# Kernel optimization log

Hardware: AMD Instinct MI355X
Metric: run time of the kernel (lower is better)

## Reference

```python
import jax, jax.numpy as jnp
import numpy as np

EPS = 1e-5

def grid_sample_bilinear(img, grid):
    """torch F.grid_sample, mode='bilinear', padding_mode='zeros', align_corners=True.
    img: (b, c, H, W); grid: (b, Hg, Wg, 2) with (x, y) in [-1, 1]. Returns (b, c, Hg, Wg)."""
    H, W = img.shape[2], img.shape[3]
    x = (grid[..., 0] + 1.0) * 0.5 * (W - 1)
    y = (grid[..., 1] + 1.0) * 0.5 * (H - 1)
    x0 = jnp.floor(x); y0 = jnp.floor(y)
    x1 = x0 + 1.0;     y1 = y0 + 1.0
    wx1 = x - x0; wx0 = 1.0 - wx1
    wy1 = y - y0; wy0 = 1.0 - wy1

    def sample_one(img_b, yi, xi):
        # img_b: (c,H,W); yi, xi: (Hg,Wg) float corner coords
        valid = ((yi >= 0) & (yi < H) & (xi >= 0) & (xi < W)).astype(img_b.dtype)
        yc = jnp.clip(yi, 0, H - 1).astype(jnp.int32)
        xc = jnp.clip(xi, 0, W - 1).astype(jnp.int32)
        return img_b[:, yc, xc] * valid[None]  # (c,Hg,Wg)

    def per_batch(img_b, x0b, x1b, y0b, y1b, wx0b, wx1b, wy0b, wy1b):
        v = (sample_one(img_b, y0b, x0b) * (wy0b * wx0b)[None]
             + sample_one(img_b, y0b, x1b) * (wy0b * wx1b)[None]
             + sample_one(img_b, y1b, x0b) * (wy1b * wx0b)[None]
             + sample_one(img_b, y1b, x1b) * (wy1b * wx1b)[None])
        return v

    return jax.vmap(per_batch)(img, x0, x1, y0, y1, wx0, wx1, wy0, wy1)


def conv_bn_relu(x, w, gamma, beta):
    # 1x1 conv (no bias) + BatchNorm2d (batch stats, training-mode forward) + ReLU
    y = jnp.einsum('nchw,oc->nohw', x, w)
    mean = y.mean(axis=(0, 2, 3), keepdims=True)
    var = y.var(axis=(0, 2, 3), keepdims=True)
    y = (y - mean) * jax.lax.rsqrt(var + EPS)
    y = y * gamma[None, :, None, None] + beta[None, :, None, None]
    return jax.nn.relu(y)


def setup_inputs() -> dict:
    key = jax.random.key(0)
    ks = jax.random.split(key, 10)
    b, c, h, w, r = 1, 128, 64, 128, 4
    d = 2 * r + 1
    f1 = jax.random.normal(ks[0], (b, c, h, w), dtype=jnp.float32)
    f2 = jax.random.normal(ks[1], (b, c, h, w), dtype=jnp.float32)
    # coords: base pixel grid (x, y) plus a small random flow perturbation
    gy, gx = jnp.meshgrid(jnp.arange(h, dtype=jnp.float32), jnp.arange(w, dtype=jnp.float32), indexing='ij')
    base = jnp.stack([gx, gy], axis=0)[None]  # (1,2,h,w)
    coords = base + 2.0 * jax.random.normal(ks[2], (b, 2, h, w), dtype=jnp.float32)
    c1, c2, c3 = 96, 128, 64
    w1 = jax.random.normal(ks[3], (c1, 2 * c), dtype=jnp.float32) * 0.05
    w2 = jax.random.normal(ks[4], (c2, c1), dtype=jnp.float32) * 0.05
    w3 = jax.random.normal(ks[5], (c3, c2), dtype=jnp.float32) * 0.05
    w4 = jax.random.normal(ks[6], (1, c3), dtype=jnp.float32) * 0.05
    b4 = jnp.zeros((1,), dtype=jnp.float32)
    g1 = jnp.ones((c1,), jnp.float32); be1 = jnp.zeros((c1,), jnp.float32)
    g2 = jnp.ones((c2,), jnp.float32); be2 = jnp.zeros((c2,), jnp.float32)
    g3 = jnp.ones((c3,), jnp.float32); be3 = jnp.zeros((c3,), jnp.float32)
    # DAP: identity init + small noise so gradients are non-trivial
    wdap = jnp.eye(d * d, dtype=jnp.float32) + 0.01 * jax.random.normal(ks[7], (d * d, d * d), dtype=jnp.float32)
    return {"f1": f1, "f2": f2, "coords": coords,
            "w1": w1, "g1": g1, "be1": be1,
            "w2": w2, "g2": g2, "be2": be2,
            "w3": w3, "g3": g3, "be3": be3,
            "w4": w4, "b4": b4, "wdap": wdap, "radius": 4}


def reference(f1, f2, coords, w1, g1, be1, w2, g2, be2, w3, g3, be3, w4, b4, wdap, radius):
    b, c, h, w = f1.shape
    r = radius
    d = 2 * r + 1
    dx = jnp.linspace(-r, r, d, dtype=f1.dtype)
    delta = jnp.stack(jnp.meshgrid(dx, dx, indexing='ij'), axis=-1)  # (d,d,2)
    coords_p = jnp.transpose(coords, (0, 2, 3, 1))  # (b,h,w,2)
    cent = coords_p[:, None, :, None, :, :] + delta.reshape(1, d, 1, d, 1, 2)  # (b,d,h,d,w,2)
    cx = 2.0 * cent[..., 0] / (w - 1) - 1.0
    cy = 2.0 * cent[..., 1] / (h - 1) - 1.0
    grid = jnp.stack([cx, cy], axis=-1).reshape(b, d * h, d * w, 2)
    f2s = grid_sample_bilinear(f2, grid)                     # (b,c,d*h,d*w)
    f2s = f2s.reshape(b, c, d, h, d, w).transpose(0, 2, 4, 1, 3, 5)  # (b,d,d,c,h,w)
    f1e = jnp.broadcast_to(f1[:, None, None], (b, d, d, c, h, w))
    corr = jnp.concatenate([f1e, f2s], axis=3).reshape(b * d * d, 2 * c, h, w)
    x = conv_bn_relu(corr, w1, g1, be1)
    x = conv_bn_relu(x, w2, g2, be2)
    x = conv_bn_relu(x, w3, g3, be3)
    cost = jnp.einsum('nchw,oc->nohw', x, w4) + b4[None, :, None, None]  # (b*d*d,1,h,w)
    cost = cost.reshape(b, d * d, h, w)
    # DAP: 1x1 conv over the d*d displacement channels, no bias
    cost = jnp.einsum('bkhw,lk->blhw', cost, wdap)
    return cost  # (b, (2r+1)^2, h, w)
```

## Files before the change

### kernel.cpp

```cpp
#include <hip/hip_runtime.h>
#include <hip/hip_bf16.h>

#define H 64
#define W 128
#define P 8192
#define DD 81
#define NS 663552
#define C1 96
#define C2 128
#define C3 64
#define EPSF 1e-5f
#define NSLOT 128

#define X1S 104
#define X2S 136
#define X1TS 136

#define NGB 324
#define NGSLOT 8

typedef __attribute__((ext_vector_type(8))) short bf16x8;
typedef __attribute__((ext_vector_type(4))) float f32x4;

#define S1SUM 0
#define S1SSQ (S1SUM + NSLOT * C1)
#define M1SUM (S1SSQ + NSLOT * C1)
#define S3SUM (M1SUM + NSLOT * C1)
#define S3SSQ (S3SUM + NSLOT * C3)
#define GSLOT (S3SSQ + NSLOT * C3)
#define STATS_ZERO_FLOATS (GSLOT + NGSLOT * 9216)
#define S1Sc 126976
#define S1Tc (S1Sc + C1)
#define S2Sc (S1Tc + C1)
#define S2Tc (S2Sc + C2)
#define S3Sc (S2Tc + C2)
#define S3Tc (S3Sc + C3)
#define GOFF 127552
#define COST_OFF (GOFF + 9216)
#define FLOAT_END (COST_OFF + NS)
#define A_BYTE   ((size_t)FLOAT_END * 4)
#define G_BYTE   (A_BYTE + (size_t)P * 96 * 2)
#define W2BF_BYTE (G_BYTE + (size_t)P * 96 * 2)
#define W3BF_BYTE (W2BF_BYTE + (size_t)C2 * C1 * 2)
#define Y1_BYTE  (W3BF_BYTE + (size_t)C3 * C2 * 2)
#define Y3_BYTE  (Y1_BYTE + (size_t)NS * C1 * 2)
#define WS_NEEDED (Y3_BYTE + (size_t)NS * C3 * 2)

__device__ __forceinline__ float bflo(unsigned u) { return __uint_as_float(u << 16); }
__device__ __forceinline__ float bfhi(unsigned u) { return __uint_as_float(u & 0xffff0000u); }
__device__ __forceinline__ float bfu(unsigned short v) { return __uint_as_float((unsigned)v << 16); }

__device__ __forceinline__ unsigned pkbf(float a, float b) {
  __hip_bfloat162 h = __float22bfloat162_rn(make_float2(a, b));
  unsigned u; __builtin_memcpy(&u, &h, 4);
  return u;
}

__global__ __launch_bounds__(256) void k_prep(const float* __restrict__ f1,
                                              const float* __restrict__ f2,
                                              const float* __restrict__ w1,
                                              unsigned short* __restrict__ aT,
                                              unsigned short* __restrict__ gT) {
  __shared__ float tile[128][64];
  int t = threadIdx.x;
  int p0 = blockIdx.x * 64;
  int px = t & 63, q = t >> 6;
  int c0 = q * 24;
  for (int pass = 0; pass < 2; ++pass) {
    const float* src = pass ? f2 : f1;
    unsigned short* dst = pass ? gT : aT;
    int koff = pass ? 128 : 0;
    __syncthreads();
    for (int idx = t; idx < 8192; idx += 256) {
      int kk = idx >> 6, xx = idx & 63;
      tile[kk][xx] = src[kk * P + p0 + xx];
    }
    __syncthreads();
    float acc[24];
#pragma unroll
    for (int i = 0; i < 24; ++i) acc[i] = 0.f;
    for (int kk = 0; kk < 128; ++kk) {
      float fv = tile[kk][px];
#pragma unroll
      for (int i = 0; i < 24; ++i)
        acc[i] += w1[(c0 + i) * 256 + koff + kk] * fv;
    }
#pragma unroll
    for (int i = 0; i < 24; i += 4) {
      uint2 pk;
      pk.x = pkbf(acc[i + 0], acc[i + 1]);
      pk.y = pkbf(acc[i + 2], acc[i + 3]);
      *(uint2*)(dst + ((size_t)((c0 + i) >> 2) * P + p0 + px) * 4) = pk;
    }
  }
}

__global__ void k_wprep(const float* __restrict__ w2, const float* __restrict__ w3,
                        unsigned short* __restrict__ w2bf, unsigned short* __restrict__ w3bf) {
  int idx = blockIdx.x * 256 + threadIdx.x;
  if (idx < C2 * C1) {
    w2bf[idx] = (unsigned short)(pkbf(w2[idx], 0.f) & 0xffffu);
  } else if (idx < C2 * C1 + C3 * C2) {
    w3bf[idx - C2 * C1] = (unsigned short)(pkbf(w3[idx - C2 * C1], 0.f) & 0xffffu);
  }
}

__global__ __launch_bounds__(256) void k_sample(const float* __restrict__ coords,
                                                float* __restrict__ ws,
                                                const unsigned short* __restrict__ aT,
                                                const unsigned short* __restrict__ gT,
                                                unsigned short* __restrict__ y1T) {
  int t = threadIdx.x, b = blockIdx.x;
  int cg = b % 6;
  int ptile = b / 6;
  int c = cg * 4 + (t >> 6);
  int px = t & 63;
  int p = ptile * 64 + px;
  float cx = coords[p], cy = coords[P + p];
  float fx0 = floorf(cx), fy0 = floorf(cy);
  float wx1 = cx - fx0, wx0 = 1.f - wx1;
  float wy1 = cy - fy0, wy0 = 1.f - wy1;
  int ixb = (int)fx0 - 4, iyb = (int)fy0 - 4;
  int colOff[10];
  float vx[10];
#pragma unroll
  for (int j = 0; j < 10; ++j) {
    int ix = ixb + j;
    vx[j] = (ix >= 0 && ix < W) ? 1.f : 0.f;
    colOff[j] = min(max(ix, 0), W - 1);
  }
  float ewx0[9], ewx1[9];
#pragma unroll
  for (int j = 0; j < 9; ++j) { ewx0[j] = wx0 * vx[j]; ewx1[j] = wx1 * vx[j + 1]; }
  int rowOff[10];
  float vy[10];
#pragma unroll
  for (int dy = 0; dy < 10; ++dy) {
    int iy = iyb + dy;
    vy[dy] = (iy >= 0 && iy < H) ? 1.f : 0.f;
    rowOff[dy] = min(max(iy, 0), H - 1) * W;
  }
  float ewy0[9], ewy1[9];
#pragma unroll
  for (int d = 0; d < 9; ++d) { ewy0[d] = wy0 * vy[d]; ewy1[d] = wy1 * vy[d + 1]; }
  float av[4];
  {
    uint2 a2 = *(const uint2*)(aT + ((size_t)c * P + p) * 4);
    av[0] = bflo(a2.x); av[1] = bfhi(a2.x); av[2] = bflo(a2.y); av[3] = bfhi(a2.y);
  }
  const unsigned short* gc = gT + (size_t)c * P * 4;
  float Hb[2][9][4];
  float sum[4] = {0.f, 0.f, 0.f, 0.f}, ssq[4] = {0.f, 0.f, 0.f, 0.f};
#pragma unroll
  for (int dy = 0; dy < 10; ++dy) {
    const int cur = dy & 1, prv = cur ^ 1;
    uint2 gv[10];
    const unsigned short* grow = gc + (size_t)rowOff[dy] * 4;
#pragma unroll
    for (int j = 0; j < 10; ++j) gv[j] = *(const uint2*)(grow + colOff[j] * 4);
#pragma unroll
    for (int j = 0; j < 9; ++j) {
      Hb[cur][j][0] = fmaf(ewx1[j], bflo(gv[j + 1].x), ewx0[j] * bflo(gv[j].x));
      Hb[cur][j][1] = fmaf(ewx1[j], bfhi(gv[j + 1].x), ewx0[j] * bfhi(gv[j].x));
      Hb[cur][j][2] = fmaf(ewx1[j], bflo(gv[j + 1].y), ewx0[j] * bflo(gv[j].y));
      Hb[cur][j][3] = fmaf(ewx1[j], bfhi(gv[j + 1].y), ewx0[j] * bfhi(gv[j].y));
    }
    if (dy >= 1) {
      const int dyk = dy - 1;
      float e0 = ewy0[dyk], e1 = ewy1[dyk];
#pragma unroll
      for (int j = 0; j < 9; ++j) {
        float o0 = fmaf(e0, Hb[prv][j][0], fmaf(e1, Hb[cur][j][0], av[0]));
        float o1 = fmaf(e0, Hb[prv][j][1], fmaf(e1, Hb[cur][j][1], av[1]));
        float o2 = fmaf(e0, Hb[prv][j][2], fmaf(e1, Hb[cur][j][2], av[2]));
        float o3 = fmaf(e0, Hb[prv][j][3], fmaf(e1, Hb[cur][j][3], av[3]));
        sum[0] += o0; ssq[0] = fmaf(o0, o0, ssq[0]);
        sum[1] += o1; ssq[1] = fmaf(o1, o1, ssq[1]);
        sum[2] += o2; ssq[2] = fmaf(o2, o2, ssq[2]);
        sum[3] += o3; ssq[3] = fmaf(o3, o3, ssq[3]);
        uint2 pk;
        pk.x = pkbf(o0, o1);
        pk.y = pkbf(o2, o3);
        int kk = j * 9 + dyk;
        *(uint2*)(y1T + (((size_t)kk * 24 + c) * P + p) * 4) = pk;
      }
    }
  }
#pragma unroll
  for (int m = 1; m < 64; m <<= 1) {
#pragma unroll
    for (int e = 0; e < 4; ++e) {
      sum[e] += __shfl_xor(sum[e], m);
      ssq[e] += __shfl_xor(ssq[e], m);
    }
  }
  if ((t & 63) == 0) {
    int slot = b & (NSLOT - 1);
#pragma unroll
    for (int e = 0; e < 4; ++e) {
      atomicAdd(&ws[S1SUM + slot * C1 + c * 4 + e], sum[e]);
      atomicAdd(&ws[S1SSQ + slot * C1 + c * 4 + e], ssq[e]);
    }
  }
}

__global__ void k_finalize(float* __restrict__ ws, int sumO, int ssqO,
                           const float* __restrict__ gamma, const float* __restrict__ beta,
                           int sO, int tO, int C) {
  int c = threadIdx.x;
  if (c < C) {
    float su = 0.f, sq = 0.f;
    for (int s = 0; s < NSLOT; ++s) { su += ws[sumO + s * C + c]; sq += ws[ssqO + s * C + c]; }
    float mean = su * (1.0f / (float)NS);
    float var = sq * (1.0f / (float)NS) - mean * mean;
    float sc = gamma[c] * rsqrtf(var + EPSF);
    ws[sO + c] = sc;
    ws[tO + c] = beta[c] - mean * sc;
  }
}

__global__ __launch_bounds__(256) void k_gram(const unsigned short* __restrict__ y1T,
                                              float* __restrict__ ws) {
  __shared__ unsigned short x1t[96 * X1TS];
  int t = threadIdx.x, b = blockIdx.x;
  int w = t >> 6, l = t & 63;
  int lr = l & 15, lh = l >> 4;
  int i0 = (w >> 1) * 48, j0 = (w & 1) * 48;
  f32x4 acc[9];
  f32x4 zero4 = {0.f, 0.f, 0.f, 0.f};
#pragma unroll
  for (int q = 0; q < 9; ++q) acc[q] = zero4;
  int c = t >> 3, pg = t & 7;
  float s1v[4], t1v[4];
  if (c < 24) {
#pragma unroll
    for (int e = 0; e < 4; ++e) { s1v[e] = ws[S1Sc + c * 4 + e]; t1v[e] = ws[S1Tc + c * 4 + e]; }
  }
  float msum[4] = {0.f, 0.f, 0.f, 0.f};
  for (int it = 0; it < 16; ++it) {
    int idx = b * 16 + it;
    int k = idx >> 6, p0 = (idx & 63) << 7;
    const unsigned short* y1k = y1T + (size_t)k * P * 96;
    __syncthreads();
    if (c < 24) {
      int pbase = p0 + pg * 16;
      unsigned rowu[4][8];
#pragma unroll
      for (int ii = 0; ii < 8; ++ii) {
        uint4 v = *(const uint4*)(y1k + ((size_t)c * P + pbase + ii * 2) * 4);
        float x00 = fmaxf(0.f, fmaf(s1v[0], bflo(v.x), t1v[0]));
        float x10 = fmaxf(0.f, fmaf(s1v[1], bfhi(v.x), t1v[1]));
        float x20 = fmaxf(0.f, fmaf(s1v[2], bflo(v.y), t1v[2]));
        float x30 = fmaxf(0.f, fmaf(s1v[3], bfhi(v.y), t1v[3]));
        float x01 = fmaxf(0.f, fmaf(s1v[0], bflo(v.z), t1v[0]));
        float x11 = fmaxf(0.f, fmaf(s1v[1], bfhi(v.z), t1v[1]));
        float x21 = fmaxf(0.f, fmaf(s1v[2], bflo(v.w), t1v[2]));
        float x31 = fmaxf(0.f, fmaf(s1v[3], bfhi(v.w), t1v[3]));
        msum[0] += x00 + x01; msum[1] += x10 + x11;
        msum[2] += x20 + x21; msum[3] += x30 + x31;
        rowu[0][ii] = pkbf(x00, x01);
        rowu[1][ii] = pkbf(x10, x11);
        rowu[2][ii] = pkbf(x20, x21);
        rowu[3][ii] = pkbf(x30, x31);
      }
#pragma unroll
      for (int e = 0; e < 4; ++e) {
        unsigned short* dst = x1t + (c * 4 + e) * X1TS + pg * 16;
        uint4 pk0; pk0.x = rowu[e][0]; pk0.y = rowu[e][1]; pk0.z = rowu[e][2]; pk0.w = rowu[e][3];
        uint4 pk1; pk1.x = rowu[e][4]; pk1.y = rowu[e][5]; pk1.z = rowu[e][6]; pk1.w = rowu[e][7];
        *(uint4*)dst = pk0;
        *(uint4*)(dst + 8) = pk1;
      }
    }
    __syncthreads();
#pragma unroll
    for (int kk = 0; kk < 4; ++kk) {
      bf16x8 a3[3], b3[3];
#pragma unroll
      for (int a = 0; a < 3; ++a)
        a3[a] = *(const bf16x8*)(const void*)(x1t + (i0 + a * 16 + lr) * X1TS + kk * 32 + lh * 8);
#pragma unroll
      for (int bb = 0; bb < 3; ++bb)
        b3[bb] = *(const bf16x8*)(const void*)(x1t + (j0 + bb * 16 + lr) * X1TS + kk * 32 + lh * 8);
#pragma unroll
      for (int a = 0; a < 3; ++a)
#pragma unroll
        for (int bb = 0; bb < 3; ++bb)
          acc[a * 3 + bb] = __builtin_amdgcn_mfma_f32_16x16x32_bf16(a3[a], b3[bb], acc[a * 3 + bb], 0, 0, 0);
    }
  }
  {
    float* gp = ws + GSLOT + (b & (NGSLOT - 1)) * 9216;
#pragma unroll
    for (int a = 0; a < 3; ++a)
#pragma unroll
      for (int bb = 0; bb < 3; ++bb) {
        int ti = (w >> 1) * 3 + a, tj = (w & 1) * 3 + bb;
        f32x4 v = acc[a * 3 + bb];
#pragma unroll
        for (int r = 0; r < 4; ++r)
          atomicAdd(&gp[(ti * 16 + lh * 4 + r) * 96 + tj * 16 + lr], v[r]);
      }
  }
  if (c < 24) {
#pragma unroll
    for (int m = 1; m < 8; m <<= 1)
#pragma unroll
      for (int e = 0; e < 4; ++e) msum[e] += __shfl_xor(msum[e], m);
    if (pg == 0) {
      int slot = b & (NSLOT - 1);
#pragma unroll
      for (int e = 0; e < 4; ++e) atomicAdd(&ws[M1SUM + slot * C1 + c * 4 + e], msum[e]);
    }
  }
}

__global__ void k_greduce(float* __restrict__ ws) {
  int e = blockIdx.x * 256 + threadIdx.x;
  float s = 0.f;
#pragma unroll
  for (int g = 0; g < NGSLOT; ++g) s += ws[GSLOT + g * 9216 + e];
  ws[GOFF + e] = s;
}

__global__ __launch_bounds__(256) void k_fin2g(float* __restrict__ ws,
                                               const unsigned short* __restrict__ w2bf,
                                               const float* __restrict__ g2,
                                               const float* __restrict__ be2) {
  __shared__ float wrow[96];
  __shared__ float m1f[96];
  __shared__ float red[8];
  int o = blockIdx.x, t = threadIdx.x;
  if (t < 96) {
    wrow[t] = bfu(w2bf[o * 96 + t]);
    float s = 0.f;
    for (int sl = 0; sl < NSLOT; ++sl) s += ws[M1SUM + sl * C1 + t];
    m1f[t] = s;
  }
  __syncthreads();
  float quad = 0.f;
  for (int e = t; e < 9216; e += 256) {
    int i = e / 96, j = e - i * 96;
    quad = fmaf(wrow[i] * wrow[j], ws[GOFF + e], quad);
  }
  float msm = (t < 96) ? wrow[t] * m1f[t] : 0.f;
#pragma unroll
  for (int m = 1; m < 64; m <<= 1) { quad += __shfl_xor(quad, m); msm += __shfl_xor(msm, m); }
  if ((t & 63) == 0) { red[t >> 6] = quad; red[4 + (t >> 6)] = msm; }
  __syncthreads();
  if (t == 0) {
    float q = red[0] + red[1] + red[2] + red[3];
    float mm = red[4] + red[5] + red[6] + red[7];
    float mean = mm * (1.0f / (float)NS);
    float var = q * (1.0f / (float)NS) - mean * mean;
    float sc = g2[o] * rsqrtf(var + EPSF);
    ws[S2Sc + o] = sc;
    ws[S2Tc + o] = be2[o] - mean * sc;
  }
}

__device__ __forceinline__ void build_x1(const unsigned short* __restrict__ y1k,
                                         const float* __restrict__ ws,
                                         unsigned short* lds, int p0, int t) {
  int s = t >> 1, hh = t & 1;
  int p = p0 + s;
  const float* s1p = ws + S1Sc;
  const float* t1p = ws + S1Tc;
  unsigned short* base = lds + s * X1S + hh * 48;
#pragma unroll
  for (int i2 = 0; i2 < 6; ++i2) {
    int c0 = hh * 12 + i2 * 2;
    uint2 va = *(const uint2*)(y1k + ((size_t)c0 * P + p) * 4);
    uint2 vb = *(const uint2*)(y1k + ((size_t)(c0 + 1) * P + p) * 4);
    int cb = c0 * 4;
    float x0 = fmaxf(0.f, fmaf(s1p[cb + 0], bflo(va.x), t1p[cb + 0]));
    float x1 = fmaxf(0.f, fmaf(s1p[cb + 1], bfhi(va.x), t1p[cb + 1]));
    float x2 = fmaxf(0.f, fmaf(s1p[cb + 2], bflo(va.y), t1p[cb + 2]));
    float x3 = fmaxf(0.f, fmaf(s1p[cb + 3], bfhi(va.y), t1p[cb + 3]));
    float x4 = fmaxf(0.f, fmaf(s1p[cb + 4], bflo(vb.x), t1p[cb + 4]));
    float x5 = fmaxf(0.f, fmaf(s1p[cb + 5], bfhi(vb.x), t1p[cb + 5]));
    float x6 = fmaxf(0.f, fmaf(s1p[cb + 6], bflo(vb.y), t1p[cb + 6]));
    float x7 = fmaxf(0.f, fmaf(s1p[cb + 7], bfhi(vb.y), t1p[cb + 7]));
    uint4 pk;
    pk.x = pkbf(x0, x1); pk.y = pkbf(x2, x3); pk.z = pkbf(x4, x5); pk.w = pkbf(x6, x7);
    *(uint4*)(base + i2 * 8) = pk;
  }
}

__global__ __launch_bounds__(256) void k_l23(const unsigned short* __restrict__ y1T,
                                             float* __restrict__ ws,
                                             const unsigned short* __restrict__ w2bf,
                                             const unsigned short* __restrict__ w3bf,
                                             unsigned short* __restrict__ y3T) {
  __shared__ unsigned short ldss[128 * X1S];
  int t = threadIdx.x, b = blockIdx.x;
  int k = b >> 6, p0 = (b & 63) << 7;
  size_t n0 = (size_t)k * P + p0;
  int slot = b & (NSLOT - 1);
  const unsigned short* y1k = y1T + (size_t)k * P * 96;
  build_x1(y1k, ws, ldss, p0, t);
  __syncthreads();
  int l = t & 63, wv = t >> 6;
  int o0w = wv * 32;
  int lr = l & 15, lh = l >> 4;
  bf16x8 af[2][3];
#pragma unroll
  for (int m = 0; m < 2; ++m)
#pragma unroll
    for (int kk = 0; kk < 3; ++kk)
      af[m][kk] = *(const bf16x8*)(const void*)(w2bf + (size_t)(o0w + m * 16 + lr) * 96 + kk * 32 + lh * 8);
  f32x4 acc[2][8];
  f32x4 zero4 = {0.f, 0.f, 0.f, 0.f};
#pragma unroll
  for (int m = 0; m < 2; ++m)
#pragma unroll
    for (int n = 0; n < 8; ++n) acc[m][n] = zero4;
#pragma unroll
  for (int kk = 0; kk < 3; ++kk)
#pragma unroll
    for (int n = 0; n < 8; ++n) {
      bf16x8 bfr = *(const bf16x8*)(const void*)(ldss + (n * 16 + lr) * X1S + kk * 32 + lh * 8);
      acc[0][n] = __builtin_amdgcn_mfma_f32_16x16x32_bf16(af[0][kk], bfr, acc[0][n], 0, 0, 0);
      acc[1][n] = __builtin_amdgcn_mfma_f32_16x16x32_bf16(af[1][kk], bfr, acc[1][n], 0, 0, 0);
    }
  float s2v[2][4], t2v[2][4];
#pragma unroll
  for (int m = 0; m < 2; ++m)
#pragma unroll
    for (int r = 0; r < 4; ++r) {
      int cc = o0w + m * 16 + lh * 4 + r;
      s2v[m][r] = ws[S2Sc + cc];
      t2v[m][r] = ws[S2Tc + cc];
    }
  int o2 = wv * 16;
  int ch4 = wv * 4 + lh;
  bf16x8 af2[4];
#pragma unroll
  for (int kk = 0; kk < 4; ++kk)
    af2[kk] = *(const bf16x8*)(const void*)(w3bf + (size_t)(o2 + lr) * 128 + kk * 32 + lh * 8);
  unsigned short* x2s = ldss;
  float ssum[4] = {0.f, 0.f, 0.f, 0.f}, sssq[4] = {0.f, 0.f, 0.f, 0.f};
#pragma unroll
  for (int h = 0; h < 2; ++h) {
    __syncthreads();
#pragma unroll
    for (int m = 0; m < 2; ++m)
#pragma unroll
      for (int n2 = 0; n2 < 4; ++n2) {
        f32x4 v = acc[m][h * 4 + n2];
        float x0 = fmaxf(0.f, fmaf(s2v[m][0], v[0], t2v[m][0]));
        float x1v = fmaxf(0.f, fmaf(s2v[m][1], v[1], t2v[m][1]));
        float x2v = fmaxf(0.f, fmaf(s2v[m][2], v[2], t2v[m][2]));
        float x3 = fmaxf(0.f, fmaf(s2v[m][3], v[3], t2v[m][3]));
        uint2 pk;
        pk.x = pkbf(x0, x1v);
        pk.y = pkbf(x2v, x3);
        *(uint2*)(x2s + (n2 * 16 + lr) * X2S + o0w + m * 16 + lh * 4) = pk;
      }
    __syncthreads();
    f32x4 acc2[4];
#pragma unroll
    for (int n2 = 0; n2 < 4; ++n2) acc2[n2] = zero4;
#pragma unroll
    for (int kk = 0; kk < 4; ++kk)
#pragma unroll
      for (int n2 = 0; n2 < 4; ++n2) {
        bf16x8 bfr = *(const bf16x8*)(const void*)(x2s + (n2 * 16 + lr) * X2S + kk * 32 + lh * 8);
        acc2[n2] = __builtin_amdgcn_mfma_f32_16x16x32_bf16(af2[kk], bfr, acc2[n2], 0, 0, 0);
      }
#pragma unroll
    for (int n2 = 0; n2 < 4; ++n2) {
      f32x4 v = acc2[n2];
#pragma unroll
      for (int r = 0; r < 4; ++r) { float x = v[r]; ssum[r] += x; sssq[r] = fmaf(x, x, sssq[r]); }
      uint2 pk;
      pk.x = pkbf(v[0], v[1]);
      pk.y = pkbf(v[2], v[3]);
      size_t n = n0 + h * 64 + n2 * 16 + lr;
      *(uint2*)(y3T + ((size_t)ch4 * NS + n) * 4) = pk;
    }
  }
#pragma unroll
  for (int msk = 1; msk < 16; msk <<= 1)
#pragma unroll
    for (int i = 0; i < 4; ++i) { ssum[i] += __shfl_xor(ssum[i], msk); sssq[i] += __shfl_xor(sssq[i], msk); }
  if (lr == 0) {
#pragma unroll
    for (int r = 0; r < 4; ++r) {
      int o = o2 + lh * 4 + r;
      atomicAdd(&ws[S3SUM + slot * C3 + o], ssum[r]);
      atomicAdd(&ws[S3SSQ + slot * C3 + o], sssq[r]);
    }
  }
}

__global__ __launch_bounds__(256) void k_layer4(const unsigned short* __restrict__ y3T,
                                                float* __restrict__ ws,
                                                const float* __restrict__ w4,
                                                const float* __restrict__ b4) {
  size_t n = (size_t)blockIdx.x * 256 + threadIdx.x;
  const float* s3p = ws + S3Sc;
  const float* t3p = ws + S3Tc;
  float acc = 0.f;
#pragma unroll
  for (int c16 = 0; c16 < 16; ++c16) {
    uint2 v = *(const uint2*)(y3T + ((size_t)c16 * NS + n) * 4);
    int c = c16 * 4;
    acc += fmaxf(0.f, fmaf(s3p[c + 0], bflo(v.x), t3p[c + 0])) * w4[c + 0];
    acc += fmaxf(0.f, fmaf(s3p[c + 1], bfhi(v.x), t3p[c + 1])) * w4[c + 1];
    acc += fmaxf(0.f, fmaf(s3p[c + 2], bflo(v.y), t3p[c + 2])) * w4[c + 2];
    acc += fmaxf(0.f, fmaf(s3p[c + 3], bfhi(v.y), t3p[c + 3])) * w4[c + 3];
  }
  ws[COST_OFF + n] = acc + b4[0];
}

__global__ __launch_bounds__(256) void k_dap(const float* __restrict__ ws,
                                             const float* __restrict__ wdap,
                                             float* __restrict__ out) {
  __shared__ float wd[DD * DD];
  int t = threadIdx.x;
  for (int i = t; i < DD * DD; i += 256) wd[i] = wdap[i];
  __syncthreads();
  int p = blockIdx.x * 32 + (t & 31);
  int lg = t >> 5;
  const float* cost = ws + COST_OFF;
  float cr[81];
#pragma unroll
  for (int kk = 0; kk < 81; ++kk) cr[kk] = cost[kk * P + p];
  for (int l = lg; l < 81; l += 8) {
    float acc = 0.f;
#pragma unroll
    for (int kk = 0; kk < 81; ++kk) acc = fmaf(wd[l * 81 + kk], cr[kk], acc);
    out[(size_t)l * P + p] = acc;
  }
}

__global__ void k_marker(float* out) { out[0] = 1.0e30f; }

extern "C" void kernel_launch(void* const* d_in, const int* in_sizes, int n_in,
                              void* d_out, int out_size, void* d_ws, size_t ws_size,
                              hipStream_t stream) {
  const float* f1 = (const float*)d_in[0];
  const float* f2 = (const float*)d_in[1];
  const float* coords = (const float*)d_in[2];
  const float* w1 = (const float*)d_in[3];
  const float* g1 = (const float*)d_in[4];
  const float* be1 = (const float*)d_in[5];
  const float* w2 = (const float*)d_in[6];
  const float* g2 = (const float*)d_in[7];
  const float* be2 = (const float*)d_in[8];
  const float* w3 = (const float*)d_in[9];
  const float* g3 = (const float*)d_in[10];
  const float* be3 = (const float*)d_in[11];
  const float* w4 = (const float*)d_in[12];
  const float* b4 = (const float*)d_in[13];
  const float* wdap = (const float*)d_in[14];
  float* out = (float*)d_out;
  float* ws = (float*)d_ws;

  if (ws_size < WS_NEEDED) {
    k_marker<<<1, 1, 0, stream>>>(out);
    return;
  }
  unsigned short* aT = (unsigned short*)((char*)d_ws + A_BYTE);
  unsigned short* gT = (unsigned short*)((char*)d_ws + G_BYTE);
  unsigned short* w2bf = (unsigned short*)((char*)d_ws + W2BF_BYTE);
  unsigned short* w3bf = (unsigned short*)((char*)d_ws + W3BF_BYTE);
  unsigned short* y1T = (unsigned short*)((char*)d_ws + Y1_BYTE);
  unsigned short* y3T = (unsigned short*)((char*)d_ws + Y3_BYTE);

  hipMemsetAsync(d_ws, 0, (size_t)STATS_ZERO_FLOATS * 4, stream);
  k_prep<<<128, 256, 0, stream>>>(f1, f2, w1, aT, gT);
  k_wprep<<<80, 256, 0, stream>>>(w2, w3, w2bf, w3bf);
  k_sample<<<768, 256, 0, stream>>>(coords, ws, aT, gT, y1T);
  k_finalize<<<1, 128, 0, stream>>>(ws, S1SUM, S1SSQ, g1, be1, S1Sc, S1Tc, C1);
  k_gram<<<NGB, 256, 0, stream>>>(y1T, ws);
  k_greduce<<<36, 256, 0, stream>>>(ws);
  k_fin2g<<<128, 256, 0, stream>>>(ws, w2bf, g2, be2);
  k_l23<<<5184, 256, 0, stream>>>(y1T, ws, w2bf, w3bf, y3T);
  k_finalize<<<1, 128, 0, stream>>>(ws, S3SUM, S3SSQ, g3, be3, S3Sc, S3Tc, C3);
  k_layer4<<<2592, 256, 0, stream>>>(y3T, ws, w4, b4);
  k_dap<<<256, 256, 0, stream>>>(ws, wdap, out);
}
```

Baseline: 294.1 us.

## Fuse layer4 into DAP kernel, split sample channels finer, quadruple gram blocks

Merges the final 64-to-1 projection into the DAP kernel, so the cost map goes through shared memory and is never written to or read back from global workspace. k_sample now handles two channels per thread instead of four and launches twice as many blocks with a launch-bounds occupancy hint. This cuts register pressure, at the price of narrower 4-byte gathers and stores. k_gram is launched with four times as many blocks, each doing a quarter of the iterations, to improve parallelism. The fused DAP kernel uses only 256 blocks to read all of y3T, which may under-occupy the GPU compared with the old 2592-block layer4 kernel.

```diff
diff --git a/kernel.cpp b/kernel.cpp
--- a/kernel.cpp
+++ b/kernel.cpp
@@ -16,7 +16,7 @@
 #define X2S 136
 #define X1TS 136
 
-#define NGB 324
+#define NGB 1296
 #define NGSLOT 8
 
 typedef __attribute__((ext_vector_type(8))) short bf16x8;
@@ -36,8 +36,7 @@
 #define S3Sc (S2Tc + C2)
 #define S3Tc (S3Sc + C3)
 #define GOFF 127552
-#define COST_OFF (GOFF + 9216)
-#define FLOAT_END (COST_OFF + NS)
+#define FLOAT_END (GOFF + 9216)
 #define A_BYTE   ((size_t)FLOAT_END * 4)
 #define G_BYTE   (A_BYTE + (size_t)P * 96 * 2)
 #define W2BF_BYTE (G_BYTE + (size_t)P * 96 * 2)
@@ -105,15 +104,16 @@
   }
 }
 
-__global__ __launch_bounds__(256) void k_sample(const float* __restrict__ coords,
-                                                float* __restrict__ ws,
-                                                const unsigned short* __restrict__ aT,
-                                                const unsigned short* __restrict__ gT,
-                                                unsigned short* __restrict__ y1T) {
+__global__ __launch_bounds__(256, 4) void k_sample(const float* __restrict__ coords,
+                                                   float* __restrict__ ws,
+                                                   const unsigned short* __restrict__ aT,
+                                                   const unsigned short* __restrict__ gT,
+                                                   unsigned short* __restrict__ y1T) {
   int t = threadIdx.x, b = blockIdx.x;
-  int cg = b % 6;
-  int ptile = b / 6;
-  int c = cg * 4 + (t >> 6);
+  int c2g = b % 12;
+  int ptile = b / 12;
+  int c2 = c2g * 4 + (t >> 6);
+  int c4 = c2 >> 1, hl = c2 & 1;
   int px = t & 63;
   int p = ptile * 64 + px;
   float cx = coords[p], cy = coords[P + p];
@@ -132,75 +132,56 @@
   float ewx0[9], ewx1[9];
 #pragma unroll
   for (int j = 0; j < 9; ++j) { ewx0[j] = wx0 * vx[j]; ewx1[j] = wx1 * vx[j + 1]; }
-  int rowOff[10];
-  float vy[10];
-#pragma unroll
-  for (int dy = 0; dy < 10; ++dy) {
-    int iy = iyb + dy;
-    vy[dy] = (iy >= 0 && iy < H) ? 1.f : 0.f;
-    rowOff[dy] = min(max(iy, 0), H - 1) * W;
-  }
-  float ewy0[9], ewy1[9];
-#pragma unroll
-  for (int d = 0; d < 9; ++d) { ewy0[d] = wy0 * vy[d]; ewy1[d] = wy1 * vy[d + 1]; }
-  float av[4];
+  float av0, av1;
   {
-    uint2 a2 = *(const uint2*)(aT + ((size_t)c * P + p) * 4);
-    av[0] = bflo(a2.x); av[1] = bfhi(a2.x); av[2] = bflo(a2.y); av[3] = bfhi(a2.y);
-  }
-  const unsigned short* gc = gT + (size_t)c * P * 4;
-  float Hb[2][9][4];
-  float sum[4] = {0.f, 0.f, 0.f, 0.f}, ssq[4] = {0.f, 0.f, 0.f, 0.f};
+    unsigned a2 = *(const unsigned*)(aT + ((size_t)c4 * P + p) * 4 + hl * 2);
+    av0 = bflo(a2); av1 = bfhi(a2);
+  }
+  const unsigned short* gc = gT + (size_t)c4 * P * 4 + hl * 2;
+  unsigned short* yb = y1T + (size_t)c4 * P * 4 + (size_t)p * 4 + hl * 2;
+  float Hb[2][9][2];
+  float sum0 = 0.f, sum1 = 0.f, ssq0 = 0.f, ssq1 = 0.f;
+  float vyPrev = 0.f;
 #pragma unroll
   for (int dy = 0; dy < 10; ++dy) {
     const int cur = dy & 1, prv = cur ^ 1;
-    uint2 gv[10];
-    const unsigned short* grow = gc + (size_t)rowOff[dy] * 4;
-#pragma unroll
-    for (int j = 0; j < 10; ++j) gv[j] = *(const uint2*)(grow + colOff[j] * 4);
+    int iy = iyb + dy;
+    float vy = (iy >= 0 && iy < H) ? 1.f : 0.f;
+    const unsigned short* grow = gc + (size_t)(min(max(iy, 0), H - 1) * W) * 4;
+    unsigned gv[10];
+#pragma unroll
+    for (int j = 0; j < 10; ++j) gv[j] = *(const unsigned*)(grow + colOff[j] * 4);
 #pragma unroll
     for (int j = 0; j < 9; ++j) {
-      Hb[cur][j][0] = fmaf(ewx1[j], bflo(gv[j + 1].x), ewx0[j] * bflo(gv[j].x));
-      Hb[cur][j][1] = fmaf(ewx1[j], bfhi(gv[j + 1].x), ewx0[j] * bfhi(gv[j].x));
-      Hb[cur][j][2] = fmaf(ewx1[j], bflo(gv[j + 1].y), ewx0[j] * bflo(gv[j].y));
-      Hb[cur][j][3] = fmaf(ewx1[j], bfhi(gv[j + 1].y), ewx0[j] * bfhi(gv[j].y));
+      Hb[cur][j][0] = fmaf(ewx1[j], bflo(gv[j + 1]), ewx0[j] * bflo(gv[j]));
+      Hb[cur][j][1] = fmaf(ewx1[j], bfhi(gv[j + 1]), ewx0[j] * bfhi(gv[j]));
     }
     if (dy >= 1) {
       const int dyk = dy - 1;
-      float e0 = ewy0[dyk], e1 = ewy1[dyk];
+      float e0 = wy0 * vyPrev, e1 = wy1 * vy;
 #pragma unroll
       for (int j = 0; j < 9; ++j) {
-        float o0 = fmaf(e0, Hb[prv][j][0], fmaf(e1, Hb[cur][j][0], av[0]));
-        float o1 = fmaf(e0, Hb[prv][j][1], fmaf(e1, Hb[cur][j][1], av[1]));
-        float o2 = fmaf(e0, Hb[prv][j][2], fmaf(e1, Hb[cur][j][2], av[2]));
-        float o3 = fmaf(e0, Hb[prv][j][3], fmaf(e1, Hb[cur][j][3], av[3]));
-        sum[0] += o0; ssq[0] = fmaf(o0, o0, ssq[0]);
-        sum[1] += o1; ssq[1] = fmaf(o1, o1, ssq[1]);
-        sum[2] += o2; ssq[2] = fmaf(o2, o2, ssq[2]);
-        sum[3] += o3; ssq[3] = fmaf(o3, o3, ssq[3]);
-        uint2 pk;
-        pk.x = pkbf(o0, o1);
-        pk.y = pkbf(o2, o3);
+        float o0 = fmaf(e0, Hb[prv][j][0], fmaf(e1, Hb[cur][j][0], av0));
+        float o1 = fmaf(e0, Hb[prv][j][1], fmaf(e1, Hb[cur][j][1], av1));
+        sum0 += o0; ssq0 = fmaf(o0, o0, ssq0);
+        sum1 += o1; ssq1 = fmaf(o1, o1, ssq1);
         int kk = j * 9 + dyk;
-        *(uint2*)(y1T + (((size_t)kk * 24 + c) * P + p) * 4) = pk;
+        *(unsigned*)(yb + (size_t)kk * 24 * P * 4) = pkbf(o0, o1);
       }
     }
+    vyPrev = vy;
   }
 #pragma unroll
   for (int m = 1; m < 64; m <<= 1) {
-#pragma unroll
-    for (int e = 0; e < 4; ++e) {
-      sum[e] += __shfl_xor(sum[e], m);
-      ssq[e] += __shfl_xor(ssq[e], m);
-    }
+    sum0 += __shfl_xor(sum0, m); ssq0 += __shfl_xor(ssq0, m);
+    sum1 += __shfl_xor(sum1, m); ssq1 += __shfl_xor(ssq1, m);
   }
   if ((t & 63) == 0) {
     int slot = b & (NSLOT - 1);
-#pragma unroll
-    for (int e = 0; e < 4; ++e) {
-      atomicAdd(&ws[S1SUM + slot * C1 + c * 4 + e], sum[e]);
-      atomicAdd(&ws[S1SSQ + slot * C1 + c * 4 + e], ssq[e]);
-    }
+    atomicAdd(&ws[S1SUM + slot * C1 + c2 * 2 + 0], sum0);
+    atomicAdd(&ws[S1SUM + slot * C1 + c2 * 2 + 1], sum1);
+    atomicAdd(&ws[S1SSQ + slot * C1 + c2 * 2 + 0], ssq0);
+    atomicAdd(&ws[S1SSQ + slot * C1 + c2 * 2 + 1], ssq1);
   }
 }
 
@@ -237,8 +218,8 @@
     for (int e = 0; e < 4; ++e) { s1v[e] = ws[S1Sc + c * 4 + e]; t1v[e] = ws[S1Tc + c * 4 + e]; }
   }
   float msum[4] = {0.f, 0.f, 0.f, 0.f};
-  for (int it = 0; it < 16; ++it) {
-    int idx = b * 16 + it;
+  for (int it = 0; it < 4; ++it) {
+    int idx = b * 4 + it;
     int k = idx >> 6, p0 = (idx & 63) << 7;
     const unsigned short* y1k = y1T + (size_t)k * P * 96;
     __syncthreads();
@@ -494,44 +475,49 @@
   }
 }
 
-__global__ __launch_bounds__(256) void k_layer4(const unsigned short* __restrict__ y3T,
-                                                float* __restrict__ ws,
-                                                const float* __restrict__ w4,
-                                                const float* __restrict__ b4) {
-  size_t n = (size_t)blockIdx.x * 256 + threadIdx.x;
-  const float* s3p = ws + S3Sc;
-  const float* t3p = ws + S3Tc;
-  float acc = 0.f;
-#pragma unroll
-  for (int c16 = 0; c16 < 16; ++c16) {
-    uint2 v = *(const uint2*)(y3T + ((size_t)c16 * NS + n) * 4);
-    int c = c16 * 4;
-    acc += fmaxf(0.f, fmaf(s3p[c + 0], bflo(v.x), t3p[c + 0])) * w4[c + 0];
-    acc += fmaxf(0.f, fmaf(s3p[c + 1], bfhi(v.x), t3p[c + 1])) * w4[c + 1];
-    acc += fmaxf(0.f, fmaf(s3p[c + 2], bflo(v.y), t3p[c + 2])) * w4[c + 2];
-    acc += fmaxf(0.f, fmaf(s3p[c + 3], bfhi(v.y), t3p[c + 3])) * w4[c + 3];
-  }
-  ws[COST_OFF + n] = acc + b4[0];
-}
-
-__global__ __launch_bounds__(256) void k_dap(const float* __restrict__ ws,
-                                             const float* __restrict__ wdap,
-                                             float* __restrict__ out) {
+__global__ __launch_bounds__(256) void k_dap4(const unsigned short* __restrict__ y3T,
+                                              const float* __restrict__ ws,
+                                              const float* __restrict__ w4,
+                                              const float* __restrict__ b4,
+                                              const float* __restrict__ wdap,
+                                              float* __restrict__ out) {
   __shared__ float wd[DD * DD];
+  __shared__ float cs[DD][33];
+  __shared__ float coef[3][64];
   int t = threadIdx.x;
+  int p0 = blockIdx.x * 32;
   for (int i = t; i < DD * DD; i += 256) wd[i] = wdap[i];
+  if (t < 64) {
+    coef[0][t] = ws[S3Sc + t];
+    coef[1][t] = ws[S3Tc + t];
+    coef[2][t] = w4[t];
+  }
   __syncthreads();
-  int p = blockIdx.x * 32 + (t & 31);
-  int lg = t >> 5;
-  const float* cost = ws + COST_OFF;
-  float cr[81];
-#pragma unroll
-  for (int kk = 0; kk < 81; ++kk) cr[kk] = cost[kk * P + p];
-  for (int l = lg; l < 81; l += 8) {
+  float b4v = b4[0];
+  int px = t & 31, kg = t >> 5;
+  for (int k = kg; k < DD; k += 8) {
+    size_t n = (size_t)k * P + p0 + px;
     float acc = 0.f;
 #pragma unroll
-    for (int kk = 0; kk < 81; ++kk) acc = fmaf(wd[l * 81 + kk], cr[kk], acc);
-    out[(size_t)l * P + p] = acc;
+    for (int c16 = 0; c16 < 16; ++c16) {
+      uint2 v = *(const uint2*)(y3T + ((size_t)c16 * NS + n) * 4);
+      int c = c16 * 4;
+      acc += fmaxf(0.f, fmaf(coef[0][c + 0], bflo(v.x), coef[1][c + 0])) * coef[2][c + 0];
+      acc += fmaxf(0.f, fmaf(coef[0][c + 1], bfhi(v.x), coef[1][c + 1])) * coef[2][c + 1];
+      acc += fmaxf(0.f, fmaf(coef[0][c + 2], bflo(v.y), coef[1][c + 2])) * coef[2][c + 2];
+      acc += fmaxf(0.f, fmaf(coef[0][c + 3], bfhi(v.y), coef[1][c + 3])) * coef[2][c + 3];
+    }
+    cs[k][px] = acc + b4v;
+  }
+  __syncthreads();
+  float cr[DD];
+#pragma unroll
+  for (int kk = 0; kk < DD; ++kk) cr[kk] = cs[kk][px];
+  for (int l = kg; l < DD; l += 8) {
+    float acc = 0.f;
+#pragma unroll
+    for (int kk = 0; kk < DD; ++kk) acc = fmaf(wd[l * 81 + kk], cr[kk], acc);
+    out[(size_t)l * P + p0 + px] = acc;
   }
 }
 
@@ -572,13 +558,12 @@
   hipMemsetAsync(d_ws, 0, (size_t)STATS_ZERO_FLOATS * 4, stream);
   k_prep<<<128, 256, 0, stream>>>(f1, f2, w1, aT, gT);
   k_wprep<<<80, 256, 0, stream>>>(w2, w3, w2bf, w3bf);
-  k_sample<<<768, 256, 0, stream>>>(coords, ws, aT, gT, y1T);
+  k_sample<<<1536, 256, 0, stream>>>(coords, ws, aT, gT, y1T);
   k_finalize<<<1, 128, 0, stream>>>(ws, S1SUM, S1SSQ, g1, be1, S1Sc, S1Tc, C1);
   k_gram<<<NGB, 256, 0, stream>>>(y1T, ws);
   k_greduce<<<36, 256, 0, stream>>>(ws);
   k_fin2g<<<128, 256, 0, stream>>>(ws, w2bf, g2, be2);
   k_l23<<<5184, 256, 0, stream>>>(y1T, ws, w2bf, w3bf, y3T);
   k_finalize<<<1, 128, 0, stream>>>(ws, S3SUM, S3SSQ, g3, be3, S3Sc, S3Tc, C3);
-  k_layer4<<<2592, 256, 0, stream>>>(y3T, ws, w4, b4);
-  k_dap<<<256, 256, 0, stream>>>(ws, wdap, out);
-}
+  k_dap4<<<256, 256, 0, stream>>>(y3T, ws, w4, b4, wdap, out);
+}
```

Result: slower. 349.9 us (+19.0%).
